# Kernel tuning notes

Measured on AMD Instinct MI355X. Metric: run time of the kernel, lower is better.

The kernel has to match this reference:

```python
import jax, jax.numpy as jnp
import numpy as np

C = 256
NUM_HEADS = 8
HEAD_DIM = C // NUM_HEADS
EPS = 1e-5


def setup_inputs() -> dict:
    key = jax.random.key(0)
    ks = jax.random.split(key, 12)
    b, h, w = 8, 64, 64
    s = 1.0 / np.sqrt(C)
    return {
        "cortical": jax.random.normal(ks[0], (b, C, h, w), jnp.float32),
        "subcortical": jax.random.normal(ks[1], (b, C, h, w), jnp.float32),
        "ventricular": jax.random.normal(ks[2], (b, C, h, w), jnp.float32),
        "in_proj_w": jax.random.uniform(ks[3], (3 * C, C), jnp.float32, -s, s),
        "in_proj_b": jnp.zeros((3 * C,), jnp.float32),
        "out_proj_w": jax.random.uniform(ks[4], (C, C), jnp.float32, -s, s),
        "out_proj_b": jnp.zeros((C,), jnp.float32),
        "ln_gamma": jnp.ones((C,), jnp.float32),
        "ln_beta": jnp.zeros((C,), jnp.float32),
        "conv_w": jax.random.uniform(ks[5], (C, 3 * C), jnp.float32, -1.0 / np.sqrt(3 * C), 1.0 / np.sqrt(3 * C)),
        "conv_b": jnp.zeros((C,), jnp.float32),
    }


def _forward(cortical, subcortical, ventricular,
             in_proj_w, in_proj_b, out_proj_w, out_proj_b,
             ln_gamma, ln_beta, conv_w, conv_b):
    b, c, h, w = cortical.shape
    # stack regions -> tokens of seq_len 3: (b,h,w,3,c) -> (N,3,c)
    regions = jnp.stack([cortical, subcortical, ventricular], axis=1)  # (b,3,c,h,w)
    x = regions.transpose(0, 3, 4, 1, 2).reshape(b * h * w, 3, c)
    # fused QKV projection
    qkv = x @ in_proj_w.T + in_proj_b  # (N,3,3c)
    q, k, v = jnp.split(qkv, 3, axis=-1)
    # split heads: (N,3,H,D)
    def heads(t):
        return t.reshape(-1, 3, NUM_HEADS, HEAD_DIM)
    q, k, v = heads(q), heads(k), heads(v)
    scores = jnp.einsum("nshd,nthd->nhst", q, k) / np.sqrt(HEAD_DIM)
    attn = jax.nn.softmax(scores, axis=-1)
    o = jnp.einsum("nhst,nthd->nshd", attn, v).reshape(-1, 3, c)
    o = o @ out_proj_w.T + out_proj_b
    # residual + LayerNorm over channels
    y = o + x
    mu = y.mean(-1, keepdims=True)
    var = y.var(-1, keepdims=True)
    y = (y - mu) * jax.lax.rsqrt(var + EPS) * ln_gamma + ln_beta
    # (N,3,c) -> (b,h,w,3c) region-major == torch cat along channel dim
    fused = y.reshape(b, h, w, 3 * c)
    out = fused @ conv_w.T + conv_b  # 1x1 conv as matmul
    return out.transpose(0, 3, 1, 2)  # (b,c,h,w)


def reference(cortical, subcortical, ventricular, in_proj_w, in_proj_b,
              out_proj_w, out_proj_b, ln_gamma, ln_beta, conv_w, conv_b):
    return _forward(cortical, subcortical, ventricular, in_proj_w, in_proj_b,
                    out_proj_w, out_proj_b, ln_gamma, ln_beta, conv_w, conv_b)
```

## Files before the change

### kernel.cpp

```cpp
#include <hip/hip_runtime.h>

typedef __bf16 bf16x8 __attribute__((ext_vector_type(8)));
typedef __bf16 bf16x4 __attribute__((ext_vector_type(4)));
typedef float  f32x4  __attribute__((ext_vector_type(4)));

#define XOFF   0
#define QKVOFF 49152
#define OOFF   69120
#define PSOFF  75264
#define PQOFF  76800
#define MUOFF  78336
#define RSOFF  78720
#define SMEM_BYTES 79104

static __device__ __forceinline__ unsigned short f2b(float f) {
  __bf16 h = (__bf16)f;
  return __builtin_bit_cast(unsigned short, h);
}

__global__ void convert_weights(const float* __restrict__ w_in,
                                const float* __restrict__ w_out,
                                const float* __restrict__ w_conv,
                                __bf16* __restrict__ ws) {
  int gid = blockIdx.x * 256 + threadIdx.x;
  int i4 = gid * 4;
  const float* src;
  int off;
  if (i4 < 196608)      { src = w_in;   off = i4; }
  else if (i4 < 262144) { src = w_out;  off = i4 - 196608; }
  else                  { src = w_conv; off = i4 - 262144; }
  float4 f = *(const float4*)(src + off);
  ws[i4 + 0] = (__bf16)f.x;
  ws[i4 + 1] = (__bf16)f.y;
  ws[i4 + 2] = (__bf16)f.z;
  ws[i4 + 3] = (__bf16)f.w;
}

__global__ __launch_bounds__(256, 2) void crf_fused(
    const float* __restrict__ cort,
    const float* __restrict__ subc,
    const float* __restrict__ vent,
    const __bf16* __restrict__ w_in,
    const float* __restrict__ b_in,
    const __bf16* __restrict__ w_out,
    const float* __restrict__ b_out,
    const float* __restrict__ gamma,
    const float* __restrict__ beta,
    const __bf16* __restrict__ w_conv,
    const float* __restrict__ b_conv,
    float* __restrict__ out) {
  extern __shared__ char smem[];
  const int tid  = threadIdx.x;
  const int lane = tid & 63;
  const int wv   = tid >> 6;
  const int l15  = lane & 15;
  const int l4   = lane >> 4;
  const int blk  = blockIdx.x;
  const int img  = blk >> 7;
  const int pixbase = (blk & 127) << 5;
  const size_t base = (size_t)img * (256 * 4096) + pixbase;

  {
    const float* rp0 = cort + base;
    const float* rp1 = subc + base;
    const float* rp2 = vent + base;
#pragma unroll
    for (int si = 0; si < 3; ++si) {
      const float* rp = (si == 0) ? rp0 : (si == 1) ? rp1 : rp2;
#pragma unroll
      for (int t = 0; t < 16; ++t) {
        int idx = t * 256 + tid;
        int p   = idx & 31;
        int c   = (idx >> 5) * 2;
        float f0 = rp[(size_t)c * 4096 + p];
        float f1 = rp[(size_t)(c + 1) * 4096 + p];
        int m = si * 32 + p;
        unsigned off = ((unsigned)(m * 512 + c * 2)) ^ ((unsigned)(m & 7) << 4);
        unsigned pack = (unsigned)f2b(f0) | ((unsigned)f2b(f1) << 16);
        *(unsigned*)(smem + XOFF + off) = pack;
      }
    }
  }

  f32x4 accY[6][4] = {};

  __syncthreads();

  const int wm = wv >> 1;
  const int wn = wv & 1;

  for (int h = 0; h < 8; ++h) {
    {
      f32x4 accQ[3][3] = {};
#pragma unroll
      for (int ks = 0; ks < 8; ++ks) {
        int k0 = ks * 32;
        bf16x8 af[3], bfr[3];
#pragma unroll
        for (int i = 0; i < 3; ++i) {
          int m = (wm * 3 + i) * 16 + l15;
          int kk = k0 + l4 * 8;
          unsigned off = ((unsigned)(m * 512 + kk * 2)) ^ ((unsigned)(m & 7) << 4);
          af[i] = *(const bf16x8*)(smem + XOFF + off);
        }
#pragma unroll
        for (int j = 0; j < 3; ++j) {
          int tn = wn * 3 + j;
          int jb = (tn >> 1) * 256 + h * 32 + (tn & 1) * 16;
          bfr[j] = *(const bf16x8*)(w_in + (size_t)(jb + l15) * 256 + k0 + l4 * 8);
        }
#pragma unroll
        for (int i = 0; i < 3; ++i)
#pragma unroll
          for (int j = 0; j < 3; ++j)
            accQ[i][j] = __builtin_amdgcn_mfma_f32_16x16x32_bf16(af[i], bfr[j], accQ[i][j], 0, 0, 0);
      }
#pragma unroll
      for (int j = 0; j < 3; ++j) {
        int tn = wn * 3 + j;
        int jb = (tn >> 1) * 256 + h * 32 + (tn & 1) * 16;
        float bias = b_in[jb + l15];
        int n = tn * 16 + l15;
#pragma unroll
        for (int i = 0; i < 3; ++i)
#pragma unroll
          for (int r = 0; r < 4; ++r) {
            int m = (wm * 3 + i) * 16 + l4 * 4 + r;
            *(__bf16*)(smem + QKVOFF + (m * 104 + n) * 2) = (__bf16)(accQ[i][j][r] + bias);
          }
      }
    }
    __syncthreads();

    {
      int p  = tid >> 3;
      int sl = tid & 7;
      float qf[3][4], kf[3][4], vf[3][4];
#pragma unroll
      for (int s = 0; s < 3; ++s) {
        const char* row = smem + QKVOFF + (s * 32 + p) * 208;
        bf16x4 q4 = *(const bf16x4*)(row + sl * 8);
        bf16x4 k4 = *(const bf16x4*)(row + 64 + sl * 8);
        bf16x4 v4 = *(const bf16x4*)(row + 128 + sl * 8);
#pragma unroll
        for (int d = 0; d < 4; ++d) {
          qf[s][d] = (float)q4[d];
          kf[s][d] = (float)k4[d];
          vf[s][d] = (float)v4[d];
        }
      }
      float sc[3][3];
#pragma unroll
      for (int s = 0; s < 3; ++s)
#pragma unroll
        for (int t2 = 0; t2 < 3; ++t2) {
          float d0 = qf[s][0]*kf[t2][0] + qf[s][1]*kf[t2][1] + qf[s][2]*kf[t2][2] + qf[s][3]*kf[t2][3];
          d0 += __shfl_xor(d0, 1);
          d0 += __shfl_xor(d0, 2);
          d0 += __shfl_xor(d0, 4);
          sc[s][t2] = d0 * 0.17677669529663687f;
        }
      float ov[3][4];
#pragma unroll
      for (int s = 0; s < 3; ++s) {
        float mx = fmaxf(sc[s][0], fmaxf(sc[s][1], sc[s][2]));
        float e0 = __expf(sc[s][0] - mx);
        float e1 = __expf(sc[s][1] - mx);
        float e2 = __expf(sc[s][2] - mx);
        float inv = 1.f / (e0 + e1 + e2);
        e0 *= inv; e1 *= inv; e2 *= inv;
#pragma unroll
        for (int d = 0; d < 4; ++d)
          ov[s][d] = e0 * vf[0][d] + e1 * vf[1][d] + e2 * vf[2][d];
      }
#pragma unroll
      for (int s = 0; s < 3; ++s) {
        int m = s * 32 + p;
        bf16x4 o4;
#pragma unroll
        for (int d = 0; d < 4; ++d) o4[d] = (__bf16)ov[s][d];
        unsigned off = ((unsigned)(m * 64 + sl * 8)) ^ ((unsigned)(m & 7) << 4);
        *(bf16x4*)(smem + OOFF + off) = o4;
      }
    }
    __syncthreads();

    {
      bf16x8 af[6], bfr[4];
#pragma unroll
      for (int i = 0; i < 6; ++i) {
        int m = i * 16 + l15;
        unsigned off = ((unsigned)(m * 64 + l4 * 16)) ^ ((unsigned)(m & 7) << 4);
        af[i] = *(const bf16x8*)(smem + OOFF + off);
      }
#pragma unroll
      for (int j = 0; j < 4; ++j) {
        int jr = (wv * 4 + j) * 16 + l15;
        bfr[j] = *(const bf16x8*)(w_out + (size_t)jr * 256 + h * 32 + l4 * 8);
      }
#pragma unroll
      for (int i = 0; i < 6; ++i)
#pragma unroll
        for (int j = 0; j < 4; ++j)
          accY[i][j] = __builtin_amdgcn_mfma_f32_16x16x32_bf16(af[i], bfr[j], accY[i][j], 0, 0, 0);
    }
    __syncthreads();
  }

  float bo[4], gg[4], bb[4];
#pragma unroll
  for (int j = 0; j < 4; ++j) {
    int jc = (wv * 4 + j) * 16 + l15;
    bo[j] = b_out[jc];
    gg[j] = gamma[jc];
    bb[j] = beta[jc];
  }
#pragma unroll
  for (int i = 0; i < 6; ++i)
#pragma unroll
    for (int r = 0; r < 4; ++r) {
      int m = i * 16 + l4 * 4 + r;
      float s1 = 0.f, s2 = 0.f;
#pragma unroll
      for (int j = 0; j < 4; ++j) {
        int jc = (wv * 4 + j) * 16 + l15;
        unsigned xo = ((unsigned)(m * 512 + jc * 2)) ^ ((unsigned)(m & 7) << 4);
        float xv = (float)(*(const __bf16*)(smem + XOFF + xo));
        float v = accY[i][j][r] + bo[j] + xv;
        accY[i][j][r] = v;
        s1 += v;
        s2 += v * v;
      }
      s1 += __shfl_xor(s1, 1); s2 += __shfl_xor(s2, 1);
      s1 += __shfl_xor(s1, 2); s2 += __shfl_xor(s2, 2);
      s1 += __shfl_xor(s1, 4); s2 += __shfl_xor(s2, 4);
      s1 += __shfl_xor(s1, 8); s2 += __shfl_xor(s2, 8);
      if (l15 == 0) {
        *(float*)(smem + PSOFF + (m * 4 + wv) * 4) = s1;
        *(float*)(smem + PQOFF + (m * 4 + wv) * 4) = s2;
      }
    }
  __syncthreads();
  if (tid < 96) {
    float s = 0.f, q = 0.f;
#pragma unroll
    for (int j = 0; j < 4; ++j) {
      s += *(const float*)(smem + PSOFF + (tid * 4 + j) * 4);
      q += *(const float*)(smem + PQOFF + (tid * 4 + j) * 4);
    }
    float mu  = s * (1.f / 256.f);
    float var = q * (1.f / 256.f) - mu * mu;
    *(float*)(smem + MUOFF + tid * 4) = mu;
    *(float*)(smem + RSOFF + tid * 4) = rsqrtf(var + 1e-5f);
  }
  __syncthreads();
#pragma unroll
  for (int i = 0; i < 6; ++i)
#pragma unroll
    for (int r = 0; r < 4; ++r) {
      int m = i * 16 + l4 * 4 + r;
      float mu = *(const float*)(smem + MUOFF + m * 4);
      float rs = *(const float*)(smem + RSOFF + m * 4);
      int s = m >> 5, p = m & 31;
#pragma unroll
      for (int j = 0; j < 4; ++j) {
        int jc = (wv * 4 + j) * 16 + l15;
        float yv = (accY[i][j][r] - mu) * rs * gg[j] + bb[j];
        int kk = s * 256 + jc;
        unsigned off = ((unsigned)(p * 1536 + kk * 2)) ^ ((unsigned)(p & 7) << 4);
        *(__bf16*)(smem + XOFF + off) = (__bf16)yv;
      }
    }
  __syncthreads();

  {
    f32x4 accC[4][2] = {};
#pragma unroll 4
    for (int ks = 0; ks < 24; ++ks) {
      int k0 = ks * 32;
      bf16x8 af[4], bfr2[2];
#pragma unroll
      for (int i = 0; i < 4; ++i) {
        int co = (wv * 4 + i) * 16 + l15;
        af[i] = *(const bf16x8*)(w_conv + (size_t)co * 768 + k0 + l4 * 8);
      }
#pragma unroll
      for (int j = 0; j < 2; ++j) {
        int p = j * 16 + l15;
        int kk = k0 + l4 * 8;
        unsigned off = ((unsigned)(p * 1536 + kk * 2)) ^ ((unsigned)(p & 7) << 4);
        bfr2[j] = *(const bf16x8*)(smem + XOFF + off);
      }
#pragma unroll
      for (int i = 0; i < 4; ++i)
#pragma unroll
        for (int j = 0; j < 2; ++j)
          accC[i][j] = __builtin_amdgcn_mfma_f32_16x16x32_bf16(af[i], bfr2[j], accC[i][j], 0, 0, 0);
    }
#pragma unroll
    for (int i = 0; i < 4; ++i)
#pragma unroll
      for (int r = 0; r < 4; ++r) {
        int co = (wv * 4 + i) * 16 + l4 * 4 + r;
        float cb = b_conv[co];
#pragma unroll
        for (int j = 0; j < 2; ++j) {
          int pix = pixbase + j * 16 + l15;
          out[((size_t)img * 256 + co) * 4096 + pix] = accC[i][j][r] + cb;
        }
      }
  }
}

extern "C" void kernel_launch(void* const* d_in, const int* in_sizes, int n_in,
                              void* d_out, int out_size, void* d_ws, size_t ws_size,
                              hipStream_t stream) {
  (void)in_sizes; (void)n_in; (void)out_size; (void)ws_size;
  const float* cort    = (const float*)d_in[0];
  const float* subc    = (const float*)d_in[1];
  const float* vent    = (const float*)d_in[2];
  const float* w_in_f  = (const float*)d_in[3];
  const float* b_in    = (const float*)d_in[4];
  const float* w_out_f = (const float*)d_in[5];
  const float* b_out   = (const float*)d_in[6];
  const float* gamma   = (const float*)d_in[7];
  const float* beta    = (const float*)d_in[8];
  const float* w_conv_f= (const float*)d_in[9];
  const float* b_conv  = (const float*)d_in[10];

  __bf16* ws = (__bf16*)d_ws;
  convert_weights<<<448, 256, 0, stream>>>(w_in_f, w_out_f, w_conv_f, ws);
  crf_fused<<<1024, 256, SMEM_BYTES, stream>>>(
      cort, subc, vent,
      ws,            b_in,
      ws + 196608,   b_out,
      gamma,         beta,
      ws + 262144,   b_conv,
      (float*)d_out);
}
```

Baseline: 212.0 us.

## Assign heads per wave, do attention in registers, halve pixel tile

Each block now handles 16 pixels instead of 32, and each wave computes QKV for two whole heads. Attention is done directly on the MFMA accumulators with cross-lane shuffles rather than through a shared QKV staging buffer, and the out-projection runs as one GEMM after all heads. This removes the per-head barriers and the per-head out-projection passes, and the smaller shared-memory footprint lets three blocks fit per CU. In exchange, each block reloads the weights for half as many pixels, which doubles global weight traffic and lowers MFMA reuse in the conv GEMM.

Result: slower. 360.5 us (+70.0%).

```diff
diff --git a/kernel.cpp b/kernel.cpp
--- a/kernel.cpp
+++ b/kernel.cpp
@@ -1,17 +1,15 @@
 #include <hip/hip_runtime.h>
 
 typedef __bf16 bf16x8 __attribute__((ext_vector_type(8)));
-typedef __bf16 bf16x4 __attribute__((ext_vector_type(4)));
 typedef float  f32x4  __attribute__((ext_vector_type(4)));
 
-#define XOFF   0
-#define QKVOFF 49152
-#define OOFF   69120
-#define PSOFF  75264
-#define PQOFF  76800
-#define MUOFF  78336
-#define RSOFF  78720
-#define SMEM_BYTES 79104
+#define XOFF 0
+#define OOFF 24576
+#define PSOFF 49152
+#define PQOFF 49920
+#define MUOFF 50688
+#define RSOFF 50880
+#define SMEM_BYTES 51072
 
 static __device__ __forceinline__ unsigned short f2b(float f) {
   __bf16 h = (__bf16)f;
@@ -36,7 +34,7 @@
   ws[i4 + 3] = (__bf16)f.w;
 }
 
-__global__ __launch_bounds__(256, 2) void crf_fused(
+__global__ __launch_bounds__(256, 3) void crf_fused(
     const float* __restrict__ cort,
     const float* __restrict__ subc,
     const float* __restrict__ vent,
@@ -56,8 +54,8 @@
   const int l15  = lane & 15;
   const int l4   = lane >> 4;
   const int blk  = blockIdx.x;
-  const int img  = blk >> 7;
-  const int pixbase = (blk & 127) << 5;
+  const int img  = blk >> 8;
+  const int pixbase = (blk & 255) << 4;
   const size_t base = (size_t)img * (256 * 4096) + pixbase;
 
   {
@@ -68,162 +66,144 @@
     for (int si = 0; si < 3; ++si) {
       const float* rp = (si == 0) ? rp0 : (si == 1) ? rp1 : rp2;
 #pragma unroll
-      for (int t = 0; t < 16; ++t) {
+      for (int t = 0; t < 8; ++t) {
         int idx = t * 256 + tid;
-        int p   = idx & 31;
-        int c   = (idx >> 5) * 2;
+        int p   = idx & 15;
+        int c   = (idx >> 4) * 2;
         float f0 = rp[(size_t)c * 4096 + p];
         float f1 = rp[(size_t)(c + 1) * 4096 + p];
-        int m = si * 32 + p;
+        int m = si * 16 + p;
         unsigned off = ((unsigned)(m * 512 + c * 2)) ^ ((unsigned)(m & 7) << 4);
         unsigned pack = (unsigned)f2b(f0) | ((unsigned)f2b(f1) << 16);
         *(unsigned*)(smem + XOFF + off) = pack;
       }
     }
   }
-
-  f32x4 accY[6][4] = {};
-
-  __syncthreads();
-
-  const int wm = wv >> 1;
-  const int wn = wv & 1;
-
-  for (int h = 0; h < 8; ++h) {
-    {
-      f32x4 accQ[3][3] = {};
-#pragma unroll
-      for (int ks = 0; ks < 8; ++ks) {
-        int k0 = ks * 32;
-        bf16x8 af[3], bfr[3];
-#pragma unroll
-        for (int i = 0; i < 3; ++i) {
-          int m = (wm * 3 + i) * 16 + l15;
-          int kk = k0 + l4 * 8;
-          unsigned off = ((unsigned)(m * 512 + kk * 2)) ^ ((unsigned)(m & 7) << 4);
-          af[i] = *(const bf16x8*)(smem + XOFF + off);
+  __syncthreads();
+
+  const float SC = 0.17677669529663687f;
+  for (int hh = 0; hh < 2; ++hh) {
+    const int h = wv * 2 + hh;
+    f32x4 acc[3][6] = {};
+#pragma unroll
+    for (int ks = 0; ks < 8; ++ks) {
+      const int k0 = ks * 32;
+      bf16x8 af[3], bfr[6];
+#pragma unroll
+      for (int i = 0; i < 3; ++i) {
+        int m = i * 16 + l15;
+        unsigned off = ((unsigned)(m * 512 + (k0 + l4 * 8) * 2)) ^ ((unsigned)(m & 7) << 4);
+        af[i] = *(const bf16x8*)(smem + XOFF + off);
+      }
+#pragma unroll
+      for (int j = 0; j < 6; ++j) {
+        int jb = (j >> 1) * 256 + h * 32 + (j & 1) * 16 + l15;
+        bfr[j] = *(const bf16x8*)(w_in + (size_t)jb * 256 + k0 + l4 * 8);
+      }
+#pragma unroll
+      for (int i = 0; i < 3; ++i)
+#pragma unroll
+        for (int j = 0; j < 6; ++j)
+          acc[i][j] = __builtin_amdgcn_mfma_f32_16x16x32_bf16(af[i], bfr[j], acc[i][j], 0, 0, 0);
+    }
+    float bq[2], bk[2], bv[2];
+#pragma unroll
+    for (int jq = 0; jq < 2; ++jq) {
+      bq[jq] = b_in[h * 32 + jq * 16 + l15];
+      bk[jq] = b_in[256 + h * 32 + jq * 16 + l15];
+      bv[jq] = b_in[512 + h * 32 + jq * 16 + l15];
+    }
+    float qb[3][2][4], kb[3][2][4], vb[3][2][4];
+#pragma unroll
+    for (int s = 0; s < 3; ++s)
+#pragma unroll
+      for (int jq = 0; jq < 2; ++jq)
+#pragma unroll
+        for (int r = 0; r < 4; ++r) {
+          qb[s][jq][r] = acc[s][jq][r] + bq[jq];
+          kb[s][jq][r] = acc[s][2 + jq][r] + bk[jq];
+          vb[s][jq][r] = acc[s][4 + jq][r] + bv[jq];
         }
-#pragma unroll
-        for (int j = 0; j < 3; ++j) {
-          int tn = wn * 3 + j;
-          int jb = (tn >> 1) * 256 + h * 32 + (tn & 1) * 16;
-          bfr[j] = *(const bf16x8*)(w_in + (size_t)(jb + l15) * 256 + k0 + l4 * 8);
-        }
-#pragma unroll
-        for (int i = 0; i < 3; ++i)
-#pragma unroll
-          for (int j = 0; j < 3; ++j)
-            accQ[i][j] = __builtin_amdgcn_mfma_f32_16x16x32_bf16(af[i], bfr[j], accQ[i][j], 0, 0, 0);
-      }
-#pragma unroll
-      for (int j = 0; j < 3; ++j) {
-        int tn = wn * 3 + j;
-        int jb = (tn >> 1) * 256 + h * 32 + (tn & 1) * 16;
-        float bias = b_in[jb + l15];
-        int n = tn * 16 + l15;
-#pragma unroll
-        for (int i = 0; i < 3; ++i)
-#pragma unroll
-          for (int r = 0; r < 4; ++r) {
-            int m = (wm * 3 + i) * 16 + l4 * 4 + r;
-            *(__bf16*)(smem + QKVOFF + (m * 104 + n) * 2) = (__bf16)(accQ[i][j][r] + bias);
-          }
-      }
-    }
-    __syncthreads();
-
-    {
-      int p  = tid >> 3;
-      int sl = tid & 7;
-      float qf[3][4], kf[3][4], vf[3][4];
-#pragma unroll
-      for (int s = 0; s < 3; ++s) {
-        const char* row = smem + QKVOFF + (s * 32 + p) * 208;
-        bf16x4 q4 = *(const bf16x4*)(row + sl * 8);
-        bf16x4 k4 = *(const bf16x4*)(row + 64 + sl * 8);
-        bf16x4 v4 = *(const bf16x4*)(row + 128 + sl * 8);
-#pragma unroll
-        for (int d = 0; d < 4; ++d) {
-          qf[s][d] = (float)q4[d];
-          kf[s][d] = (float)k4[d];
-          vf[s][d] = (float)v4[d];
-        }
-      }
-      float sc[3][3];
-#pragma unroll
-      for (int s = 0; s < 3; ++s)
-#pragma unroll
-        for (int t2 = 0; t2 < 3; ++t2) {
-          float d0 = qf[s][0]*kf[t2][0] + qf[s][1]*kf[t2][1] + qf[s][2]*kf[t2][2] + qf[s][3]*kf[t2][3];
-          d0 += __shfl_xor(d0, 1);
-          d0 += __shfl_xor(d0, 2);
-          d0 += __shfl_xor(d0, 4);
-          sc[s][t2] = d0 * 0.17677669529663687f;
-        }
-      float ov[3][4];
-#pragma unroll
-      for (int s = 0; s < 3; ++s) {
-        float mx = fmaxf(sc[s][0], fmaxf(sc[s][1], sc[s][2]));
-        float e0 = __expf(sc[s][0] - mx);
-        float e1 = __expf(sc[s][1] - mx);
-        float e2 = __expf(sc[s][2] - mx);
+    float pp[3][3][4];
+#pragma unroll
+    for (int si = 0; si < 3; ++si)
+#pragma unroll
+      for (int ti = 0; ti < 3; ++ti)
+#pragma unroll
+        for (int r = 0; r < 4; ++r)
+          pp[si][ti][r] = qb[si][0][r] * kb[ti][0][r] + qb[si][1][r] * kb[ti][1][r];
+#pragma unroll
+    for (int mask = 1; mask <= 8; mask <<= 1)
+#pragma unroll
+      for (int si = 0; si < 3; ++si)
+#pragma unroll
+        for (int ti = 0; ti < 3; ++ti)
+#pragma unroll
+          for (int r = 0; r < 4; ++r)
+            pp[si][ti][r] += __shfl_xor(pp[si][ti][r], mask);
+#pragma unroll
+    for (int r = 0; r < 4; ++r) {
+      int p = l4 * 4 + r;
+#pragma unroll
+      for (int si = 0; si < 3; ++si) {
+        float s0 = pp[si][0][r] * SC, s1 = pp[si][1][r] * SC, s2 = pp[si][2][r] * SC;
+        float mx = fmaxf(fmaxf(s0, s1), s2);
+        float e0 = __expf(s0 - mx), e1 = __expf(s1 - mx), e2 = __expf(s2 - mx);
         float inv = 1.f / (e0 + e1 + e2);
         e0 *= inv; e1 *= inv; e2 *= inv;
-#pragma unroll
-        for (int d = 0; d < 4; ++d)
-          ov[s][d] = e0 * vf[0][d] + e1 * vf[1][d] + e2 * vf[2][d];
-      }
-#pragma unroll
-      for (int s = 0; s < 3; ++s) {
-        int m = s * 32 + p;
-        bf16x4 o4;
-#pragma unroll
-        for (int d = 0; d < 4; ++d) o4[d] = (__bf16)ov[s][d];
-        unsigned off = ((unsigned)(m * 64 + sl * 8)) ^ ((unsigned)(m & 7) << 4);
-        *(bf16x4*)(smem + OOFF + off) = o4;
-      }
-    }
-    __syncthreads();
-
-    {
-      bf16x8 af[6], bfr[4];
-#pragma unroll
-      for (int i = 0; i < 6; ++i) {
-        int m = i * 16 + l15;
-        unsigned off = ((unsigned)(m * 64 + l4 * 16)) ^ ((unsigned)(m & 7) << 4);
-        af[i] = *(const bf16x8*)(smem + OOFF + off);
-      }
-#pragma unroll
-      for (int j = 0; j < 4; ++j) {
-        int jr = (wv * 4 + j) * 16 + l15;
-        bfr[j] = *(const bf16x8*)(w_out + (size_t)jr * 256 + h * 32 + l4 * 8);
-      }
-#pragma unroll
-      for (int i = 0; i < 6; ++i)
-#pragma unroll
-        for (int j = 0; j < 4; ++j)
-          accY[i][j] = __builtin_amdgcn_mfma_f32_16x16x32_bf16(af[i], bfr[j], accY[i][j], 0, 0, 0);
-    }
-    __syncthreads();
+        int m = si * 16 + p;
+#pragma unroll
+        for (int jq = 0; jq < 2; ++jq) {
+          float ov = e0 * vb[0][jq][r] + e1 * vb[1][jq][r] + e2 * vb[2][jq][r];
+          int col = h * 32 + jq * 16 + l15;
+          unsigned off = ((unsigned)(m * 512 + col * 2)) ^ ((unsigned)(m & 7) << 4);
+          *(__bf16*)(smem + OOFF + off) = (__bf16)ov;
+        }
+      }
+    }
+  }
+  __syncthreads();
+
+  f32x4 accY[3][4] = {};
+#pragma unroll
+  for (int ks = 0; ks < 8; ++ks) {
+    const int k0 = ks * 32;
+    bf16x8 af[3], bfr[4];
+#pragma unroll
+    for (int i = 0; i < 3; ++i) {
+      int m = i * 16 + l15;
+      unsigned off = ((unsigned)(m * 512 + (k0 + l4 * 8) * 2)) ^ ((unsigned)(m & 7) << 4);
+      af[i] = *(const bf16x8*)(smem + OOFF + off);
+    }
+#pragma unroll
+    for (int j = 0; j < 4; ++j) {
+      int jr = wv * 64 + j * 16 + l15;
+      bfr[j] = *(const bf16x8*)(w_out + (size_t)jr * 256 + k0 + l4 * 8);
+    }
+#pragma unroll
+    for (int i = 0; i < 3; ++i)
+#pragma unroll
+      for (int j = 0; j < 4; ++j)
+        accY[i][j] = __builtin_amdgcn_mfma_f32_16x16x32_bf16(af[i], bfr[j], accY[i][j], 0, 0, 0);
   }
 
   float bo[4], gg[4], bb[4];
 #pragma unroll
   for (int j = 0; j < 4; ++j) {
-    int jc = (wv * 4 + j) * 16 + l15;
+    int jc = wv * 64 + j * 16 + l15;
     bo[j] = b_out[jc];
     gg[j] = gamma[jc];
     bb[j] = beta[jc];
   }
 #pragma unroll
-  for (int i = 0; i < 6; ++i)
+  for (int i = 0; i < 3; ++i)
 #pragma unroll
     for (int r = 0; r < 4; ++r) {
       int m = i * 16 + l4 * 4 + r;
       float s1 = 0.f, s2 = 0.f;
 #pragma unroll
       for (int j = 0; j < 4; ++j) {
-        int jc = (wv * 4 + j) * 16 + l15;
+        int jc = wv * 64 + j * 16 + l15;
         unsigned xo = ((unsigned)(m * 512 + jc * 2)) ^ ((unsigned)(m & 7) << 4);
         float xv = (float)(*(const __bf16*)(smem + XOFF + xo));
         float v = accY[i][j][r] + bo[j] + xv;
@@ -241,7 +221,7 @@
       }
     }
   __syncthreads();
-  if (tid < 96) {
+  if (tid < 48) {
     float s = 0.f, q = 0.f;
 #pragma unroll
     for (int j = 0; j < 4; ++j) {
@@ -255,16 +235,16 @@
   }
   __syncthreads();
 #pragma unroll
-  for (int i = 0; i < 6; ++i)
+  for (int i = 0; i < 3; ++i)
 #pragma unroll
     for (int r = 0; r < 4; ++r) {
       int m = i * 16 + l4 * 4 + r;
       float mu = *(const float*)(smem + MUOFF + m * 4);
       float rs = *(const float*)(smem + RSOFF + m * 4);
-      int s = m >> 5, p = m & 31;
+      int s = m >> 4, p = m & 15;
 #pragma unroll
       for (int j = 0; j < 4; ++j) {
-        int jc = (wv * 4 + j) * 16 + l15;
+        int jc = wv * 64 + j * 16 + l15;
         float yv = (accY[i][j][r] - mu) * rs * gg[j] + bb[j];
         int kk = s * 256 + jc;
         unsigned off = ((unsigned)(p * 1536 + kk * 2)) ^ ((unsigned)(p & 7) << 4);
@@ -274,40 +254,30 @@
   __syncthreads();
 
   {
-    f32x4 accC[4][2] = {};
+    f32x4 accC[4] = {};
 #pragma unroll 4
     for (int ks = 0; ks < 24; ++ks) {
-      int k0 = ks * 32;
-      bf16x8 af[4], bfr2[2];
+      const int k0 = ks * 32;
+      bf16x8 af[4];
 #pragma unroll
       for (int i = 0; i < 4; ++i) {
-        int co = (wv * 4 + i) * 16 + l15;
+        int co = wv * 64 + i * 16 + l15;
         af[i] = *(const bf16x8*)(w_conv + (size_t)co * 768 + k0 + l4 * 8);
       }
-#pragma unroll
-      for (int j = 0; j < 2; ++j) {
-        int p = j * 16 + l15;
-        int kk = k0 + l4 * 8;
-        unsigned off = ((unsigned)(p * 1536 + kk * 2)) ^ ((unsigned)(p & 7) << 4);
-        bfr2[j] = *(const bf16x8*)(smem + XOFF + off);
-      }
+      int pb = l15;
+      unsigned off = ((unsigned)(pb * 1536 + (k0 + l4 * 8) * 2)) ^ ((unsigned)(pb & 7) << 4);
+      bf16x8 bfr = *(const bf16x8*)(smem + XOFF + off);
 #pragma unroll
       for (int i = 0; i < 4; ++i)
-#pragma unroll
-        for (int j = 0; j < 2; ++j)
-          accC[i][j] = __builtin_amdgcn_mfma_f32_16x16x32_bf16(af[i], bfr2[j], accC[i][j], 0, 0, 0);
+        accC[i] = __builtin_amdgcn_mfma_f32_16x16x32_bf16(af[i], bfr, accC[i], 0, 0, 0);
     }
 #pragma unroll
     for (int i = 0; i < 4; ++i)
 #pragma unroll
       for (int r = 0; r < 4; ++r) {
-        int co = (wv * 4 + i) * 16 + l4 * 4 + r;
+        int co = wv * 64 + i * 16 + l4 * 4 + r;
         float cb = b_conv[co];
-#pragma unroll
-        for (int j = 0; j < 2; ++j) {
-          int pix = pixbase + j * 16 + l15;
-          out[((size_t)img * 256 + co) * 4096 + pix] = accC[i][j][r] + cb;
-        }
+        out[((size_t)img * 256 + co) * 4096 + pixbase + l15] = accC[i][r] + cb;
       }
   }
 }
@@ -330,7 +300,7 @@
 
   __bf16* ws = (__bf16*)d_ws;
   convert_weights<<<448, 256, 0, stream>>>(w_in_f, w_out_f, w_conv_f, ws);
-  crf_fused<<<1024, 256, SMEM_BYTES, stream>>>(
+  crf_fused<<<2048, 256, SMEM_BYTES, stream>>>(
       cort, subc, vent,
       ws,            b_in,
       ws + 196608,   b_out,
```
